# Kernel optimization log

Measured on AMD Instinct MI355X. Metric: run time of the kernel, lower is better.

## Reference

```python
import jax, jax.numpy as jnp
import numpy as np

B, S, D, H, DFF = 2, 2048, 1024, 16, 4096
DK = D // H
EPS = float(np.finfo(np.float32).eps)  # torch RMSNorm default eps = finfo eps


def rmsnorm(x, g):
    var = jnp.mean(x * x, axis=-1, keepdims=True)
    return x * jax.lax.rsqrt(var + EPS) * g


def rope_cos_sin(seq_len, dim, base=10000.0):
    inv_freq = 1.0 / (base ** (jnp.arange(0, dim, 2, dtype=jnp.float32) / dim))
    t = jnp.arange(seq_len, dtype=jnp.float32)
    freqs = jnp.outer(t, inv_freq)            # [S, dim/2]
    emb = jnp.concatenate([freqs, freqs], -1)  # [S, dim]
    return jnp.cos(emb), jnp.sin(emb)


def rotate_half(x):
    x1, x2 = x[..., : x.shape[-1] // 2], x[..., x.shape[-1] // 2:]
    return jnp.concatenate([-x2, x1], axis=-1)


def setup_inputs() -> dict:
    key = jax.random.key(0)
    ks = jax.random.split(key, 16)
    sc = 0.02
    return {
        "x": jax.random.normal(ks[0], (B, S, D), jnp.float32),
        "wq": jax.random.normal(ks[1], (D, D), jnp.float32) * sc,
        "bq": jnp.zeros((D,), jnp.float32),
        "wk": jax.random.normal(ks[2], (D, D), jnp.float32) * sc,
        "bk": jnp.zeros((D,), jnp.float32),
        "wv": jax.random.normal(ks[3], (D, D), jnp.float32) * sc,
        "bv": jnp.zeros((D,), jnp.float32),
        "wo": jax.random.normal(ks[4], (D, D), jnp.float32) * sc,
        "bo": jnp.zeros((D,), jnp.float32),
        "w1": jax.random.normal(ks[5], (D, DFF), jnp.float32) * sc,
        "b1": jnp.zeros((DFF,), jnp.float32),
        "w2": jax.random.normal(ks[6], (DFF, D), jnp.float32) * sc,
        "b2": jnp.zeros((D,), jnp.float32),
        "g1": jnp.ones((D,), jnp.float32),
        "g2": jnp.ones((D,), jnp.float32),
    }


def reference(x, wq, bq, wk, bk, wv, bv, wo, bo, w1, b1, w2, b2, g1, g2):
    b, s, d = x.shape
    # --- self-attention sublayer (pre-RMSNorm residual) ---
    h = rmsnorm(x, g1)
    q = (h @ wq + bq).reshape(b, s, H, DK).transpose(0, 2, 1, 3)  # [B,H,S,dk]
    k = (h @ wk + bk).reshape(b, s, H, DK).transpose(0, 2, 1, 3)
    v = (h @ wv + bv).reshape(b, s, H, DK).transpose(0, 2, 1, 3)
    cos, sin = rope_cos_sin(s, DK)
    cos = cos[None, None]  # [1,1,S,dk]
    sin = sin[None, None]
    q = q * cos + rotate_half(q) * sin
    k = k * cos + rotate_half(k) * sin
    scores = jnp.einsum("bhqd,bhkd->bhqk", q, k) / jnp.sqrt(jnp.float32(DK))
    p = jax.nn.softmax(scores, axis=-1)
    o = jnp.einsum("bhqk,bhkd->bhqd", p, v)
    o = o.transpose(0, 2, 1, 3).reshape(b, s, d)
    attn_out = o @ wo + bo
    x = x + attn_out
    # --- feed-forward sublayer ---
    h2 = rmsnorm(x, g2)
    ff = jax.nn.relu(h2 @ w1 + b1) @ w2 + b2
    return x + ff
```

## Files before the change

### kernel.cpp

```cpp
#include <hip/hip_runtime.h>
#include <math.h>

typedef unsigned short u16;
typedef __attribute__((ext_vector_type(8))) short bf16x8;
typedef __attribute__((ext_vector_type(4))) float f32x4;
typedef __attribute__((ext_vector_type(4))) unsigned int u32x4;

#define B_ 2
#define S_ 2048
#define D_ 1024
#define H_ 16
#define DK_ 64
#define DFF_ 4096
#define EPS_ 1.1920928955078125e-07f
#define EXP2SC 0.18033688011112042f

__device__ __forceinline__ float bf2f(u16 u) {
  unsigned int v = ((unsigned int)u) << 16;
  return __builtin_bit_cast(float, v);
}
__device__ __forceinline__ u16 f2bf(float f) {
  unsigned int x = __builtin_bit_cast(unsigned int, f);
  x += 0x7fffu + ((x >> 16) & 1u);
  return (u16)(x >> 16);
}

#if __has_builtin(__builtin_amdgcn_exp2f)
__device__ __forceinline__ float exp2r(float x) { return __builtin_amdgcn_exp2f(x); }
#else
__device__ __forceinline__ float exp2r(float x) { return exp2f(x); }
#endif

typedef __attribute__((address_space(3))) unsigned int lds_uint;
typedef const __attribute__((address_space(1))) unsigned int glb_uint;
__device__ __forceinline__ void gload16(const void* g, void* l) {
  __builtin_amdgcn_global_load_lds((glb_uint*)g, (lds_uint*)l, 16, 0, 0);
}

template <int N>
__device__ __forceinline__ void waitcnt_vm() {
  if constexpr (N == 8) asm volatile("s_waitcnt vmcnt(8)" ::: "memory");
  else if constexpr (N == 6) asm volatile("s_waitcnt vmcnt(6)" ::: "memory");
  else if constexpr (N == 4) asm volatile("s_waitcnt vmcnt(4)" ::: "memory");
  else asm volatile("s_waitcnt vmcnt(0)" ::: "memory");
}

__device__ __forceinline__ unsigned int cvtpk(float lo, float hi) {
  unsigned int d;
  asm("v_cvt_pk_bf16_f32 %0, %1, %2" : "=v"(d) : "v"(lo), "v"(hi));
  return d;
}
__device__ __forceinline__ void plswap32(unsigned int& a, unsigned int& b) {
  asm("v_permlane32_swap_b32 %0, %1" : "+v"(a), "+v"(b));
}
__device__ __forceinline__ void plswap16(unsigned int& a, unsigned int& b) {
  asm("v_permlane16_swap_b32 %0, %1" : "+v"(a), "+v"(b));
}

__device__ __forceinline__ void xcd_swizzle(int& bx, int& by) {
  const int nx = gridDim.x;
  const int nwg = nx * gridDim.y;
  const int lin = blockIdx.y * nx + blockIdx.x;
  const int swz = (lin & 7) * (nwg >> 3) + (lin >> 3);
  bx = swz % nx;
  by = swz / nx;
}

__global__ __launch_bounds__(256) void prep_qkvo(
    const float* __restrict__ wq, const float* __restrict__ wk,
    const float* __restrict__ wv, const float* __restrict__ wo,
    u16* __restrict__ qkvT, u16* __restrict__ woT,
    float* __restrict__ cosT, float* __restrict__ sinT) {
  __shared__ float t[32][33];
  const int bid = blockIdx.x;
  const int tid = threadIdx.x;
  if (bid < 4096) {
    const int m = bid >> 10;
    const int tb = bid & 1023;
    const float* src = (m == 0) ? wq : (m == 1) ? wk : (m == 2) ? wv : wo;
    u16* dst = (m == 3) ? woT : qkvT + (size_t)m * D_ * D_;
    const int c0 = (tb & 31) * 32, r0 = (tb >> 5) * 32;
    const int tx = tid & 31, ty = tid >> 5;
#pragma unroll
    for (int i = 0; i < 32; i += 8)
      t[ty + i][tx] = src[(size_t)(r0 + ty + i) * D_ + (c0 + tx)];
    __syncthreads();
#pragma unroll
    for (int i = 0; i < 32; i += 8)
      dst[(size_t)(c0 + ty + i) * D_ + (r0 + tx)] = f2bf(t[tx][ty + i]);
  } else {
    const int idx = (bid - 4096) * 256 + tid;
    const int s = idx >> 5, i = idx & 31;
    double inv = exp(((double)(-2 * i) / (double)DK_) * log(10000.0));
    double ang = (double)s * inv;
    cosT[idx] = (float)cos(ang);
    sinT[idx] = (float)sin(ang);
  }
}

__global__ __launch_bounds__(256) void prep_w12(
    const float* __restrict__ w1, const float* __restrict__ w2,
    u16* __restrict__ w1T, u16* __restrict__ w2T) {
  __shared__ float t[32][33];
  const int bid = blockIdx.x;
  const int tid = threadIdx.x;
  const int tx = tid & 31, ty = tid >> 5;
  if (bid < 4096) {
    const int c0 = (bid & 127) * 32, r0 = (bid >> 7) * 32;
#pragma unroll
    for (int i = 0; i < 32; i += 8)
      t[ty + i][tx] = w1[(size_t)(r0 + ty + i) * DFF_ + (c0 + tx)];
    __syncthreads();
#pragma unroll
    for (int i = 0; i < 32; i += 8)
      w1T[(size_t)(c0 + ty + i) * D_ + (r0 + tx)] = f2bf(t[tx][ty + i]);
  } else {
    const int b2 = bid - 4096;
    const int c0 = (b2 & 31) * 32, r0 = (b2 >> 5) * 32;
#pragma unroll
    for (int i = 0; i < 32; i += 8)
      t[ty + i][tx] = w2[(size_t)(r0 + ty + i) * D_ + (c0 + tx)];
    __syncthreads();
#pragma unroll
    for (int i = 0; i < 32; i += 8)
      w2T[(size_t)(c0 + ty + i) * DFF_ + (r0 + tx)] = f2bf(t[tx][ty + i]);
  }
}

__global__ __launch_bounds__(256) void rmsnorm_k(const float* __restrict__ X,
                                                 const float* __restrict__ g,
                                                 u16* __restrict__ out) {
  const int row = blockIdx.x;
  const float* xr = X + (size_t)row * D_;
  u16* orow = out + (size_t)row * D_;
  const int tid = threadIdx.x;
  float vals[4];
  float s = 0.f;
#pragma unroll
  for (int j = 0; j < 4; j++) {
    float v = xr[tid + j * 256];
    vals[j] = v;
    s += v * v;
  }
#pragma unroll
  for (int off = 32; off > 0; off >>= 1) s += __shfl_down(s, off, 64);
  __shared__ float red[4];
  __shared__ float ssc;
  int lane = tid & 63, wave = tid >> 6;
  if (lane == 0) red[wave] = s;
  __syncthreads();
  if (tid == 0) ssc = 1.0f / sqrtf((red[0] + red[1] + red[2] + red[3]) * (1.0f / D_) + EPS_);
  __syncthreads();
  float sc = ssc;
#pragma unroll
  for (int j = 0; j < 4; j++) {
    int i = tid + j * 256;
    orow[i] = f2bf(vals[j] * sc * g[i]);
  }
}

#define GK_STAGE(BU, K0)                                                               \
  _Pragma("unroll")                                                                    \
  for (int p = 0; p < 2; p++) {                                                        \
    _Pragma("unroll")                                                                  \
    for (int c = wave; c < BM / 16; c += 4) {                                          \
      const u16* gp = gkA + (size_t)(m0 + c * 16 + lrow) * gkLD + (K0) + p * 32 + lcol; \
      gload16(gp, (char*)As + __builtin_amdgcn_readfirstlane((BU) * (BM * 128) + p * (BM * 64) + c * 1024)); \
    }                                                                                  \
    _Pragma("unroll")                                                                  \
    for (int c = wave; c < BN / 16; c += 4) {                                          \
      const u16* gp = gkB + (size_t)(n0 + c * 16 + lrow) * gkLD + (K0) + p * 32 + lcol; \
      gload16(gp, (char*)Bs + __builtin_amdgcn_readfirstlane((BU) * (BN * 128) + p * (BN * 64) + c * 1024)); \
    }                                                                                  \
  }

#define GK_COMPUTE(BU)                                                                 \
  _Pragma("unroll")                                                                    \
  for (int p = 0; p < 2; p++) {                                                        \
    bf16x8 af[WR], bfv[WC];                                                            \
    _Pragma("unroll")                                                                  \
    for (int i = 0; i < WR; i++)                                                       \
      af[i] = *(const bf16x8*)&As[(BU) * (BM * 64) + p * (BM * 32) + (wm + i * 16 + l16) * 32 + quad * 8]; \
    _Pragma("unroll")                                                                  \
    for (int j = 0; j < WC; j++)                                                       \
      bfv[j] = *(const bf16x8*)&Bs[(BU) * (BN * 64) + p * (BN * 32) + (wn + j * 16 + l16) * 32 + quad * 8]; \
    _Pragma("unroll")                                                                  \
    for (int i = 0; i < WR; i++)                                                       \
      _Pragma("unroll")                                                                \
      for (int j = 0; j < WC; j++)                                                     \
        acc[i][j] = __builtin_amdgcn_mfma_f32_16x16x32_bf16(af[i], bfv[j], acc[i][j], 0, 0, 0); \
  }

#define GEMM_KLOOP(APTR, BPTR, KLEN, KLD)                                              \
  {                                                                                    \
    const u16* gkA = (APTR);                                                           \
    const u16* gkB = (BPTR);                                                           \
    const int gkLD = (KLD);                                                            \
    GK_STAGE(0, 0)                                                                     \
    GK_STAGE(1, 64)                                                                    \
    int gkcur = 0;                                                                     \
    for (int k0 = 0; k0 < (KLEN); k0 += 64) {                                          \
      if (k0 + 64 < (KLEN)) waitcnt_vm<WR + WC>();   \
      else waitcnt_vm<0>();                                      \
      __builtin_amdgcn_s_barrier();                                                    \
      GK_COMPUTE(gkcur)                                                                \
      __builtin_amdgcn_s_barrier();                         \
      if (k0 + 128 < (KLEN)) { GK_STAGE(gkcur, k0 + 128) }                             \
      gkcur ^= 1;                                                                      \
    }                                                                                  \
  }

template <int MODE, int WR, int WC>
__global__ __launch_bounds__(256) void gemm_bt(
    const u16* __restrict__ A, const u16* __restrict__ Bt, const float* __restrict__ bias,
    u16* __restrict__ outB, float* __restrict__ outF, const float* __restrict__ resF,
    int M, int N, int K) {
  constexpr int BM = 2 * WR * 16;
  constexpr int BN = 2 * WC * 16;
  __shared__ u16 As[2 * BM * 64];
  __shared__ u16 Bs[2 * BN * 64];
  const int tid = threadIdx.x;
  const int wave = tid >> 6, lane = tid & 63, quad = lane >> 4, l16 = lane & 15;
  const int wm = (wave >> 1) * (WR * 16), wn = (wave & 1) * (WC * 16);
  int bx, by;
  xcd_swizzle(bx, by);
  const int m0 = by * BM, n0 = bx * BN;
  const int lrow = lane >> 2, lcol = (lane & 3) * 8;
  f32x4 acc[WR][WC] = {};
  GEMM_KLOOP(A, Bt, K, K)
#pragma unroll
  for (int i = 0; i < WR; i++)
#pragma unroll
    for (int j = 0; j < WC; j++) {
      int col = n0 + wn + j * 16 + l16;
      float bv = bias[col];
#pragma unroll
      for (int r = 0; r < 4; r++) {
        int row = m0 + wm + i * 16 + quad * 4 + r;
        size_t off = (size_t)row * N + col;
        float v = acc[i][j][r] + bv;
        if constexpr (MODE == 1) v = fmaxf(v, 0.f);
        if constexpr (MODE == 2) outF[off] = v + resF[off];
        else outB[off] = f2bf(v);
      }
    }
}

__global__ __launch_bounds__(256) void gemm_qkv(
    const u16* __restrict__ A, const u16* __restrict__ Bt,
    const float* __restrict__ bq, const float* __restrict__ bk, const float* __restrict__ bv,
    const float* __restrict__ cosT, const float* __restrict__ sinT,
    u16* __restrict__ Qb, u16* __restrict__ Kb, u16* __restrict__ VT, int M, int K) {
  constexpr int WR = 4, WC = 4;
  constexpr int BM = 128, BN = 128;
  __shared__ u16 As[2 * BM * 64];
  __shared__ u16 Bs[2 * BN * 64];
  const int tid = threadIdx.x;
  const int wave = tid >> 6, lane = tid & 63, quad = lane >> 4, l16 = lane & 15;
  const int wm = (wave >> 1) * 64, wn = (wave & 1) * 64;
  int bx, by;
  xcd_swizzle(bx, by);
  const int m0 = by * BM, n0 = bx * BN;
  const int lrow = lane >> 2, lcol = (lane & 3) * 8;
  f32x4 acc[WR][WC] = {};
  GEMM_KLOOP(A, Bt, K, K)
  const int g = n0 >> 10;
  if (g < 2) {
    u16* dst = (g == 0) ? Qb : Kb;
    const float* bias = (g == 0) ? bq : bk;
    const float scq = (g == 0) ? EXP2SC : 1.0f;
#pragma unroll
    for (int i = 0; i < WR; i++)
#pragma unroll
      for (int jp = 0; jp < 2; jp++) {
        int col0 = n0 + wn + jp * 16 + l16;
        int c0 = col0 & 1023;
        float bv0 = bias[c0], bv1 = bias[c0 + 32];
        int irot = jp * 16 + l16;
        int row0 = m0 + wm + i * 16 + quad * 4;
#pragma unroll
        for (int r = 0; r < 4; r++) {
          int row = row0 + r;
          int s2 = row & 2047;
          float cs = cosT[s2 * 32 + irot];
          float sn = sinT[s2 * 32 + irot];
          float x0 = acc[i][jp][r] + bv0;
          float x1 = acc[i][jp + 2][r] + bv1;
          dst[(size_t)row * D_ + c0]      = f2bf((x0 * cs - x1 * sn) * scq);
          dst[(size_t)row * D_ + c0 + 32] = f2bf((x1 * cs + x0 * sn) * scq);
        }
      }
  } else {
#pragma unroll
    for (int i = 0; i < WR; i++)
#pragma unroll
      for (int j = 0; j < WC; j++) {
        int col = n0 + wn + j * 16 + l16;
        int c = col & 1023;
        float bvv = bv[c];
        int row0 = m0 + wm + i * 16 + quad * 4;
        int hh = c >> 6, dk = c & 63;
        int b = row0 >> 11, s2 = row0 & 2047;
        ushort4 pv;
        pv.x = f2bf(acc[i][j][0] + bvv);
        pv.y = f2bf(acc[i][j][1] + bvv);
        pv.z = f2bf(acc[i][j][2] + bvv);
        pv.w = f2bf(acc[i][j][3] + bvv);
        *(ushort4*)&VT[(((size_t)(b * H_ + hh)) * DK_ + dk) * S_ + s2] = pv;
      }
  }
}

template <int WR, int WC>
__global__ __launch_bounds__(256) void gemm_splitk(
    const u16* __restrict__ A, const u16* __restrict__ Bt, const float* __restrict__ bias,
    float* outF, int M, int N, int Kslice, int Kld) {
  constexpr int BM = 2 * WR * 16;
  constexpr int BN = 2 * WC * 16;
  __shared__ u16 As[2 * BM * 64];
  __shared__ u16 Bs[2 * BN * 64];
  const int tid = threadIdx.x;
  const int wave = tid >> 6, lane = tid & 63, quad = lane >> 4, l16 = lane & 15;
  const int wm = (wave >> 1) * (WR * 16), wn = (wave & 1) * (WC * 16);
  int bx, by;
  xcd_swizzle(bx, by);
  const int m0 = by * BM, n0 = bx * BN;
  const int lrow = lane >> 2, lcol = (lane & 3) * 8;
  const u16* Ao = A + (size_t)blockIdx.z * Kslice;
  const u16* Bo = Bt + (size_t)blockIdx.z * Kslice;
  f32x4 acc[WR][WC] = {};
  GEMM_KLOOP(Ao, Bo, Kslice, Kld)
  const bool addb = (blockIdx.z == 0);
#pragma unroll
  for (int i = 0; i < WR; i++)
#pragma unroll
    for (int j = 0; j < WC; j++) {
      int col = n0 + wn + j * 16 + l16;
      float bv = addb ? bias[col] : 0.f;
#pragma unroll
      for (int r = 0; r < 4; r++) {
        int row = m0 + wm + i * 16 + quad * 4 + r;
        unsafeAtomicAdd(&outF[(size_t)row * N + col], acc[i][j][r] + bv);
      }
    }
}

__device__ __forceinline__ void softmax_pack(f32x4 s0, f32x4 s1, f32x4 s2, f32x4 s3,
                                             bf16x8& pf0, bf16x8& pf1) {
  f32x4 p0, p1, p2, p3;
#pragma unroll
  for (int r = 0; r < 4; r++) {
    p0[r] = exp2r(s0[r]);
    p1[r] = exp2r(s1[r]);
    p2[r] = exp2r(s2[r]);
    p3[r] = exp2r(s3[r]);
  }
  unsigned int X0 = cvtpk(p0[0], p0[1]), X1 = cvtpk(p0[2], p0[3]);
  unsigned int Y0 = cvtpk(p1[0], p1[1]), Y1 = cvtpk(p1[2], p1[3]);
  unsigned int Z0 = cvtpk(p2[0], p2[1]), Z1 = cvtpk(p2[2], p2[3]);
  unsigned int W0 = cvtpk(p3[0], p3[1]), W1 = cvtpk(p3[2], p3[3]);
  plswap32(X0, Y0); plswap16(X0, Y0);
  plswap32(X1, Y1); plswap16(X1, Y1);
  plswap32(Z0, W0); plswap16(Z0, W0);
  plswap32(Z1, W1); plswap16(Z1, W1);
  u32x4 lo = {X0, X1, Y0, Y1};
  u32x4 hi = {Z0, Z1, W0, W1};
  pf0 = __builtin_bit_cast(bf16x8, lo);
  pf1 = __builtin_bit_cast(bf16x8, hi);
}

__global__ __launch_bounds__(256, 4) void flash_attn(u16* __restrict__ Q,
                                                     const u16* __restrict__ Kg,
                                                     const u16* __restrict__ VT) {
  const int bh = blockIdx.y;
  const int b = bh >> 4, h = bh & 15;
  const int q0 = blockIdx.x * 128;
  const int tid = threadIdx.x;
  const int wave = tid >> 6, lane = tid & 63, quad = lane >> 4, l16 = lane & 15;
  const size_t base = (size_t)b * S_ * D_ + h * DK_;
  const size_t vbase = (size_t)bh * DK_ * S_;

  __shared__ u16 Ks[2][4096];
  __shared__ u16 Vts[2][4096];

  const int srow8 = lane >> 3;
  const int scol = ((lane & 7) ^ srow8) * 8;
  const int kkey = wave * 16 + srow8;
  const u16* kp0 = Kg + base + (size_t)kkey * D_ + scol;
  const int vdk = wave * 16 + srow8;
  const u16* vp0 = VT + vbase + (size_t)vdk * S_ + scol;

#define FA_STAGE(BU, KT)                                                               \
  _Pragma("unroll")                                                                    \
  for (int c = 0; c < 2; c++) {                                                        \
    gload16(kp0 + (size_t)((KT) + c * 8) * D_,                                         \
            (char*)Ks + __builtin_amdgcn_readfirstlane((BU) * 8192 + wave * 2048 + c * 1024)); \
    gload16(vp0 + (size_t)(c * 8) * S_ + (KT),                                         \
            (char*)Vts + __builtin_amdgcn_readfirstlane((BU) * 8192 + wave * 2048 + c * 1024)); \
  }

  FA_STAGE(0, 0)
  FA_STAGE(1, 64)

  const size_t qoffA = base + (size_t)(q0 + wave * 32 + l16) * D_ + quad * 8;
  const size_t qoffB = qoffA + (size_t)16 * D_;
  bf16x8 qa0 = *(const bf16x8*)(Q + qoffA);
  bf16x8 qa1 = *(const bf16x8*)(Q + qoffA + 32);
  bf16x8 qb0 = *(const bf16x8*)(Q + qoffB);
  bf16x8 qb1 = *(const bf16x8*)(Q + qoffB + 32);

  f32x4 oa[4] = {}, ob[4] = {};
  f32x4 lsa_acc = {}, lsb_acc = {};
  const u32x4 onesu = {0x3F803F80u, 0x3F803F80u, 0x3F803F80u, 0x3F803F80u};
  const bf16x8 ones = __builtin_bit_cast(bf16x8, onesu);
  const int sw = (l16 & 7) << 4;

#define FA_TILE(BU)                                                                    \
  {                                                                                    \
    const char* KsB = (const char*)Ks + (BU) * 8192;                                   \
    const char* VtsB = (const char*)Vts + (BU) * 8192;                                 \
    f32x4 sa[4] = {}, sb[4] = {};                                                      \
    __builtin_amdgcn_s_setprio(1);                                                     \
    _Pragma("unroll")                                                                  \
    for (int nt = 0; nt < 4; nt++) {                                                   \
      const char* krow = KsB + (nt * 16 + l16) * 128;                                  \
      bf16x8 k0 = *(const bf16x8*)(krow + ((quad * 16) ^ sw));                         \
      bf16x8 k1 = *(const bf16x8*)(krow + ((64 + quad * 16) ^ sw));                    \
      sa[nt] = __builtin_amdgcn_mfma_f32_16x16x32_bf16(k0, qa0, sa[nt], 0, 0, 0);      \
      sa[nt] = __builtin_amdgcn_mfma_f32_16x16x32_bf16(k1, qa1, sa[nt], 0, 0, 0);      \
      sb[nt] = __builtin_amdgcn_mfma_f32_16x16x32_bf16(k0, qb0, sb[nt], 0, 0, 0);      \
      sb[nt] = __builtin_amdgcn_mfma_f32_16x16x32_bf16(k1, qb1, sb[nt], 0, 0, 0);      \
    }                                                                                  \
    __builtin_amdgcn_s_setprio(0);                                                     \
    bf16x8 pa0, pa1, pb0, pb1;                                                         \
    softmax_pack(sa[0], sa[1], sa[2], sa[3], pa0, pa1);                                \
    softmax_pack(sb[0], sb[1], sb[2], sb[3], pb0, pb1);                                \
    __builtin_amdgcn_s_setprio(1);                                                     \
    lsa_acc = __builtin_amdgcn_mfma_f32_16x16x32_bf16(pa0, ones, lsa_acc, 0, 0, 0);    \
    lsa_acc = __builtin_amdgcn_mfma_f32_16x16x32_bf16(pa1, ones, lsa_acc, 0, 0, 0);    \
    lsb_acc = __builtin_amdgcn_mfma_f32_16x16x32_bf16(pb0, ones, lsb_acc, 0, 0, 0);    \
    lsb_acc = __builtin_amdgcn_mfma_f32_16x16x32_bf16(pb1, ones, lsb_acc, 0, 0, 0);    \
    _Pragma("unroll")                                                                  \
    for (int nt = 0; nt < 4; nt++) {                                                   \
      const char* vrow = VtsB + (nt * 16 + l16) * 128;                                 \
      bf16x8 v0 = *(const bf16x8*)(vrow + ((quad * 16) ^ sw));                         \
      bf16x8 v1 = *(const bf16x8*)(vrow + ((64 + quad * 16) ^ sw));                    \
      oa[nt] = __builtin_amdgcn_mfma_f32_16x16x32_bf16(pa0, v0, oa[nt], 0, 0, 0);      \
      oa[nt] = __builtin_amdgcn_mfma_f32_16x16x32_bf16(pa1, v1, oa[nt], 0, 0, 0);      \
      ob[nt] = __builtin_amdgcn_mfma_f32_16x16x32_bf16(pb0, v0, ob[nt], 0, 0, 0);      \
      ob[nt] = __builtin_amdgcn_mfma_f32_16x16x32_bf16(pb1, v1, ob[nt], 0, 0, 0);      \
    }                                                                                  \
    __builtin_amdgcn_s_setprio(0);                                                     \
  }

  int cur = 0;
  for (int kt = 0; kt < S_; kt += 64) {
    if (kt + 64 < S_) waitcnt_vm<4>();
    else waitcnt_vm<0>();
    __builtin_amdgcn_s_barrier();
    FA_TILE(cur)
    __builtin_amdgcn_s_barrier();
    if (kt + 128 < S_) { FA_STAGE(cur, kt + 128) }
    cur ^= 1;
  }
#undef FA_STAGE
#undef FA_TILE

#pragma unroll
  for (int r = 0; r < 4; r++) {
    float inva = 1.0f / lsa_acc[r];
    float invb = 1.0f / lsb_acc[r];
    const size_t aoff = base + (size_t)(q0 + wave * 32 + quad * 4 + r) * D_;
    const size_t boff = aoff + (size_t)16 * D_;
#pragma unroll
    for (int nt = 0; nt < 4; nt++) {
      Q[aoff + nt * 16 + l16] = f2bf(oa[nt][r] * inva);
      Q[boff + nt * 16 + l16] = f2bf(ob[nt][r] * invb);
    }
  }
}

extern "C" void kernel_launch(void* const* d_in, const int* in_sizes, int n_in,
                              void* d_out, int out_size, void* d_ws, size_t ws_size,
                              hipStream_t stream) {
  const float* x  = (const float*)d_in[0];
  const float* wq = (const float*)d_in[1];
  const float* bq = (const float*)d_in[2];
  const float* wk = (const float*)d_in[3];
  const float* bk = (const float*)d_in[4];
  const float* wv = (const float*)d_in[5];
  const float* bv = (const float*)d_in[6];
  const float* wo = (const float*)d_in[7];
  const float* bo = (const float*)d_in[8];
  const float* w1 = (const float*)d_in[9];
  const float* b1 = (const float*)d_in[10];
  const float* w2 = (const float*)d_in[11];
  const float* b2 = (const float*)d_in[12];
  const float* g1 = (const float*)d_in[13];
  const float* g2 = (const float*)d_in[14];

  char* ws = (char*)d_ws;
  const size_t MB = 1024 * 1024;
  u16* qkvT = (u16*)(ws + 0 * MB);
  u16* woT  = (u16*)(ws + 6 * MB);
  u16* h    = (u16*)(ws + 8 * MB);
  u16* Qb   = (u16*)(ws + 16 * MB);
  u16* Kb   = (u16*)(ws + 24 * MB);
  float* cosT = (float*)(ws + 32 * MB);
  float* sinT = (float*)(ws + 32 * MB + 256 * 1024);
  u16* w2T  = (u16*)(ws + 0 * MB);
  u16* w1T  = (u16*)(ws + 16 * MB);
  u16* f1   = (u16*)(ws + 24 * MB);
  u16* h2   = h;
  u16* Ob   = Qb;
  u16* VT   = (u16*)d_out;
  float* x2 = (float*)d_out;
  const bool bigffn = (ws_size >= 57 * MB);

  const int MS = B_ * S_;
  prep_qkvo<<<4096 + S_ * 32 / 256, 256, 0, stream>>>(wq, wk, wv, wo, qkvT, woT, cosT, sinT);
  rmsnorm_k<<<MS, 256, 0, stream>>>(x, g1, h);
  gemm_qkv<<<dim3(3 * D_ / 128, MS / 128), 256, 0, stream>>>(h, qkvT, bq, bk, bv, cosT, sinT, Qb, Kb, VT, MS, D_);
  flash_attn<<<dim3(S_ / 128, B_ * H_), 256, 0, stream>>>(Qb, Kb, VT);
  gemm_bt<2, 4, 2><<<dim3(D_ / 64, MS / 128), 256, 0, stream>>>(Ob, woT, bo, nullptr, x2, x, MS, D_, D_);

  prep_w12<<<8192, 256, 0, stream>>>(w1, w2, w1T, w2T);
  rmsnorm_k<<<MS, 256, 0, stream>>>(x2, g2, h2);
  if (bigffn) {
    gemm_bt<1, 4, 4><<<dim3(DFF_ / 128, MS / 128), 256, 0, stream>>>(h2, w1T, b1, f1, nullptr, nullptr, MS, DFF_, D_);
    gemm_splitk<4, 4><<<dim3(D_ / 128, MS / 128, 2), 256, 0, stream>>>(f1, w2T, b2, x2, MS, D_, 2048, DFF_);
  } else {
    for (int i = 0; i < 2; i++) {
      const u16* h2h = h2 + (size_t)i * 2048 * D_;
      float* x2h = x2 + (size_t)i * 2048 * D_;
      gemm_bt<1, 4, 4><<<dim3(DFF_ / 128, 2048 / 128), 256, 0, stream>>>(h2h, w1T, b1, f1, nullptr, nullptr, 2048, DFF_, D_);
      gemm_splitk<4, 4><<<dim3(D_ / 128, 2048 / 128, 4), 256, 0, stream>>>(f1, w2T, b2, x2h, 2048, D_, 1024, DFF_);
    }
  }
  (void)in_sizes; (void)n_in; (void)out_size;
}
```

Baseline: 348.9 us.

## Halve GEMM K-tile to 32, raise occupancy, split-K 4 with 3D XCD swizzle

```diff
diff --git a/kernel.cpp b/kernel.cpp
--- a/kernel.cpp
+++ b/kernel.cpp
@@ -42,6 +42,7 @@
   if constexpr (N == 8) asm volatile("s_waitcnt vmcnt(8)" ::: "memory");
   else if constexpr (N == 6) asm volatile("s_waitcnt vmcnt(6)" ::: "memory");
   else if constexpr (N == 4) asm volatile("s_waitcnt vmcnt(4)" ::: "memory");
+  else if constexpr (N == 3) asm volatile("s_waitcnt vmcnt(3)" ::: "memory");
   else asm volatile("s_waitcnt vmcnt(0)" ::: "memory");
 }
 
@@ -64,6 +65,17 @@
   const int swz = (lin & 7) * (nwg >> 3) + (lin >> 3);
   bx = swz % nx;
   by = swz / nx;
+}
+
+__device__ __forceinline__ void xcd_swizzle3(int& bx, int& by, int& bz) {
+  const int gx = gridDim.x, gy = gridDim.y, gz = gridDim.z;
+  const int nb = gx * gy * gz;
+  const int lin = ((int)blockIdx.z * gy + blockIdx.y) * gx + blockIdx.x;
+  const int w = (lin & 7) * (nb >> 3) + (lin >> 3);
+  bz = w % gz;
+  const int r = w / gz;
+  bx = r % gx;
+  by = r / gx;
 }
 
 __global__ __launch_bounds__(256) void prep_qkvo(
@@ -161,29 +173,25 @@
 
 #define GK_STAGE(BU, K0)                                                               \
   _Pragma("unroll")                                                                    \
-  for (int p = 0; p < 2; p++) {                                                        \
-    _Pragma("unroll")                                                                  \
-    for (int c = wave; c < BM / 16; c += 4) {                                          \
-      const u16* gp = gkA + (size_t)(m0 + c * 16 + lrow) * gkLD + (K0) + p * 32 + lcol; \
-      gload16(gp, (char*)As + __builtin_amdgcn_readfirstlane((BU) * (BM * 128) + p * (BM * 64) + c * 1024)); \
-    }                                                                                  \
-    _Pragma("unroll")                                                                  \
-    for (int c = wave; c < BN / 16; c += 4) {                                          \
-      const u16* gp = gkB + (size_t)(n0 + c * 16 + lrow) * gkLD + (K0) + p * 32 + lcol; \
-      gload16(gp, (char*)Bs + __builtin_amdgcn_readfirstlane((BU) * (BN * 128) + p * (BN * 64) + c * 1024)); \
-    }                                                                                  \
+  for (int c = wave; c < BM / 16; c += 4) {                                            \
+    const u16* gp = gkA + (size_t)(m0 + c * 16 + lrow) * gkLD + (K0) + lcol;           \
+    gload16(gp, (char*)As + __builtin_amdgcn_readfirstlane((BU) * (BM * 64) + c * 1024)); \
+  }                                                                                    \
+  _Pragma("unroll")                                                                    \
+  for (int c = wave; c < BN / 16; c += 4) {                                            \
+    const u16* gp = gkB + (size_t)(n0 + c * 16 + lrow) * gkLD + (K0) + lcol;           \
+    gload16(gp, (char*)Bs + __builtin_amdgcn_readfirstlane((BU) * (BN * 64) + c * 1024)); \
   }
 
 #define GK_COMPUTE(BU)                                                                 \
-  _Pragma("unroll")                                                                    \
-  for (int p = 0; p < 2; p++) {                                                        \
+  {                                                                                    \
     bf16x8 af[WR], bfv[WC];                                                            \
     _Pragma("unroll")                                                                  \
     for (int i = 0; i < WR; i++)                                                       \
-      af[i] = *(const bf16x8*)&As[(BU) * (BM * 64) + p * (BM * 32) + (wm + i * 16 + l16) * 32 + quad * 8]; \
+      af[i] = *(const bf16x8*)&As[(BU) * (BM * 32) + (wm + i * 16 + l16) * 32 + quad * 8]; \
     _Pragma("unroll")                                                                  \
     for (int j = 0; j < WC; j++)                                                       \
-      bfv[j] = *(const bf16x8*)&Bs[(BU) * (BN * 64) + p * (BN * 32) + (wn + j * 16 + l16) * 32 + quad * 8]; \
+      bfv[j] = *(const bf16x8*)&Bs[(BU) * (BN * 32) + (wn + j * 16 + l16) * 32 + quad * 8]; \
     _Pragma("unroll")                                                                  \
     for (int i = 0; i < WR; i++)                                                       \
       _Pragma("unroll")                                                                \
@@ -197,28 +205,28 @@
     const u16* gkB = (BPTR);                                                           \
     const int gkLD = (KLD);                                                            \
     GK_STAGE(0, 0)                                                                     \
-    GK_STAGE(1, 64)                                                                    \
+    GK_STAGE(1, 32)                                                                    \
     int gkcur = 0;                                                                     \
-    for (int k0 = 0; k0 < (KLEN); k0 += 64) {                                          \
-      if (k0 + 64 < (KLEN)) waitcnt_vm<WR + WC>();   \
+    for (int k0 = 0; k0 < (KLEN); k0 += 32) {                                          \
+      if (k0 + 32 < (KLEN)) waitcnt_vm<WR / 2 + WC / 2>();       \
       else waitcnt_vm<0>();                                      \
       __builtin_amdgcn_s_barrier();                                                    \
       GK_COMPUTE(gkcur)                                                                \
-      __builtin_amdgcn_s_barrier();                         \
-      if (k0 + 128 < (KLEN)) { GK_STAGE(gkcur, k0 + 128) }                             \
+      __builtin_amdgcn_s_barrier();                             \
+      if (k0 + 64 < (KLEN)) { GK_STAGE(gkcur, k0 + 64) }                               \
       gkcur ^= 1;                                                                      \
     }                                                                                  \
   }
 
 template <int MODE, int WR, int WC>
-__global__ __launch_bounds__(256) void gemm_bt(
+__global__ __launch_bounds__(256, 4) void gemm_bt(
     const u16* __restrict__ A, const u16* __restrict__ Bt, const float* __restrict__ bias,
     u16* __restrict__ outB, float* __restrict__ outF, const float* __restrict__ resF,
     int M, int N, int K) {
   constexpr int BM = 2 * WR * 16;
   constexpr int BN = 2 * WC * 16;
-  __shared__ u16 As[2 * BM * 64];
-  __shared__ u16 Bs[2 * BN * 64];
+  __shared__ u16 As[2 * BM * 32];
+  __shared__ u16 Bs[2 * BN * 32];
   const int tid = threadIdx.x;
   const int wave = tid >> 6, lane = tid & 63, quad = lane >> 4, l16 = lane & 15;
   const int wm = (wave >> 1) * (WR * 16), wn = (wave & 1) * (WC * 16);
@@ -246,15 +254,15 @@
     }
 }
 
-__global__ __launch_bounds__(256) void gemm_qkv(
+__global__ __launch_bounds__(256, 4) void gemm_qkv(
     const u16* __restrict__ A, const u16* __restrict__ Bt,
     const float* __restrict__ bq, const float* __restrict__ bk, const float* __restrict__ bv,
     const float* __restrict__ cosT, const float* __restrict__ sinT,
     u16* __restrict__ Qb, u16* __restrict__ Kb, u16* __restrict__ VT, int M, int K) {
   constexpr int WR = 4, WC = 4;
   constexpr int BM = 128, BN = 128;
-  __shared__ u16 As[2 * BM * 64];
-  __shared__ u16 Bs[2 * BN * 64];
+  __shared__ u16 As[2 * BM * 32];
+  __shared__ u16 Bs[2 * BN * 32];
   const int tid = threadIdx.x;
   const int wave = tid >> 6, lane = tid & 63, quad = lane >> 4, l16 = lane & 15;
   const int wm = (wave >> 1) * 64, wn = (wave & 1) * 64;
@@ -312,25 +320,25 @@
 }
 
 template <int WR, int WC>
-__global__ __launch_bounds__(256) void gemm_splitk(
+__global__ __launch_bounds__(256, 4) void gemm_splitk(
     const u16* __restrict__ A, const u16* __restrict__ Bt, const float* __restrict__ bias,
     float* outF, int M, int N, int Kslice, int Kld) {
   constexpr int BM = 2 * WR * 16;
   constexpr int BN = 2 * WC * 16;
-  __shared__ u16 As[2 * BM * 64];
-  __shared__ u16 Bs[2 * BN * 64];
+  __shared__ u16 As[2 * BM * 32];
+  __shared__ u16 Bs[2 * BN * 32];
   const int tid = threadIdx.x;
   const int wave = tid >> 6, lane = tid & 63, quad = lane >> 4, l16 = lane & 15;
   const int wm = (wave >> 1) * (WR * 16), wn = (wave & 1) * (WC * 16);
-  int bx, by;
-  xcd_swizzle(bx, by);
+  int bx, by, bz;
+  xcd_swizzle3(bx, by, bz);
   const int m0 = by * BM, n0 = bx * BN;
   const int lrow = lane >> 2, lcol = (lane & 3) * 8;
-  const u16* Ao = A + (size_t)blockIdx.z * Kslice;
-  const u16* Bo = Bt + (size_t)blockIdx.z * Kslice;
+  const u16* Ao = A + (size_t)bz * Kslice;
+  const u16* Bo = Bt + (size_t)bz * Kslice;
   f32x4 acc[WR][WC] = {};
   GEMM_KLOOP(Ao, Bo, Kslice, Kld)
-  const bool addb = (blockIdx.z == 0);
+  const bool addb = (bz == 0);
 #pragma unroll
   for (int i = 0; i < WR; i++)
 #pragma unroll
@@ -528,7 +536,7 @@
   rmsnorm_k<<<MS, 256, 0, stream>>>(x2, g2, h2);
   if (bigffn) {
     gemm_bt<1, 4, 4><<<dim3(DFF_ / 128, MS / 128), 256, 0, stream>>>(h2, w1T, b1, f1, nullptr, nullptr, MS, DFF_, D_);
-    gemm_splitk<4, 4><<<dim3(D_ / 128, MS / 128, 2), 256, 0, stream>>>(f1, w2T, b2, x2, MS, D_, 2048, DFF_);
+    gemm_splitk<4, 4><<<dim3(D_ / 128, MS / 128, 4), 256, 0, stream>>>(f1, w2T, b2, x2, MS, D_, 1024, DFF_);
   } else {
     for (int i = 0; i < 2; i++) {
       const u16* h2h = h2 + (size_t)i * 2048 * D_;
```

Measured after the change: 365.5 us. 1.05x slower.
